# Kernel tuning notes

Measured on AMD Instinct MI355X. Metric: run time of the kernel, lower is better.

The kernel has to match this reference:

```python
import jax, jax.numpy as jnp
import numpy as np

N, B = 128, 8                                # seq_len, batch
V, E, H, S, T = 32000, 256, 256, 256, 32     # vocab, embed, hidden, segment_dim, segment_threshold


def _gru_cell(x, h, Wi, Wh, bi, bh):
    # PyTorch GRU cell convention (gates ordered r,z,n)
    gi = x @ Wi.T + bi
    gh = h @ Wh.T + bh
    ir, iz, inn = jnp.split(gi, 3, axis=-1)
    hr, hz, hn = jnp.split(gh, 3, axis=-1)
    r = jax.nn.sigmoid(ir + hr)
    z = jax.nn.sigmoid(iz + hz)
    n = jnp.tanh(inn + r * hn)
    return (1.0 - z) * n + z * h


def _run_gru(xs, h0, Wi, Wh, bi, bh):
    def step(h, x):
        h = _gru_cell(x, h, Wi, Wh, bi, bh)
        return h, h
    hT, ys = jax.lax.scan(step, h0, xs)
    return ys, hT


def setup_inputs() -> dict:
    key = jax.random.key(0)
    ks = jax.random.split(key, 17)
    sc = 1.0 / np.sqrt(H).astype(np.float32)
    w = lambda k, shape: jax.random.normal(k, shape, jnp.float32) * sc
    return {
        "tokens": jax.random.randint(ks[0], (N, B), 0, V, dtype=jnp.int32),
        "emb": w(ks[1], (V, E)),
        "Wi_f": w(ks[2], (3 * H, E)), "Wh_f": w(ks[3], (3 * H, H)),
        "bi_f": w(ks[4], (3 * H,)),  "bh_f": w(ks[5], (3 * H,)),
        "Wi_r": w(ks[6], (3 * H, E)), "Wh_r": w(ks[7], (3 * H, H)),
        "bi_r": w(ks[8], (3 * H,)),  "bh_r": w(ks[9], (3 * H,)),
        "Wi_s": w(ks[10], (3 * S, 2 * H)), "Wh_s": w(ks[11], (3 * S, S)),
        "bi_s": w(ks[12], (3 * S,)), "bh_s": w(ks[13], (3 * S,)),
        # deterministic stand-ins for the per-start torch.randn initial hiddens
        "h0f": jax.random.normal(ks[14], (N, B, S), jnp.float32),
        "h0b": jax.random.normal(ks[15], (N, B, S), jnp.float32),
    }


def reference(tokens, emb, Wi_f, Wh_f, bi_f, bh_f, Wi_r, Wh_r, bi_r, bh_r,
              Wi_s, Wh_s, bi_s, bh_s, h0f, h0b):
    x = emb[tokens]                                   # (N,B,E); dropout p=0
    h0 = jnp.zeros((B, H), x.dtype)
    ys_f, _ = _run_gru(x, h0, Wi_f, Wh_f, bi_f, bh_f)
    ys_r, _ = _run_gru(x[::-1], h0, Wi_r, Wh_r, bi_r, bh_r)
    outputs = jnp.concatenate([ys_f, ys_r[::-1]], axis=-1)   # (N,B,2H)

    def seg(window, h0i):                             # window (T,B,2H)
        def step(h, xt):
            h = _gru_cell(xt, h, Wi_s, Wh_s, bi_s, bh_s)
            return h, h
        hT, ys = jax.lax.scan(step, h0i, window)
        return ys, hT

    ii = jnp.arange(N)[:, None]                       # (N,1) segment start i
    tt = jnp.arange(T)[None, :]                       # (1,T) step within window
    jf = ii + tt                                      # forward target column j
    jb = ii - tt                                      # backward target row j
    win_f = outputs[jnp.clip(jf, 0, N - 1)]           # (N,T,B,2H)
    win_b = outputs[jnp.clip(jb, 0, N - 1)]
    outs_f, _ = jax.vmap(seg)(win_f, h0f)             # (N,T,B,S)
    outs_b, hT_b = jax.vmap(seg)(win_b, h0b)

    jf_s = jnp.where(jf < N, jf, N)                   # OOB index -> dropped
    jb_s = jnp.where(jb >= 0, jb, N)
    dp_f = jnp.zeros((N, N, B, S), outputs.dtype).at[ii, jf_s].set(outs_f, mode="drop")
    dp_b = jnp.zeros((N, N, B, S), outputs.dtype).at[jb_s, ii].set(outs_b, mode="drop")
    dp = jnp.concatenate([dp_f, dp_b], axis=-1)       # (N,N,B,2S)
    rows, cols = jnp.triu_indices(N)
    dp_tri = dp[rows, cols]                           # (N*(N+1)/2, B, 2S)

    # final hiddens as the torch loops leave them: forward i=N-1 runs exactly
    # one step; backward i=N-1 runs T steps (N >= T so all in range).
    hid_f = _gru_cell(outputs[-1], h0f[-1], Wi_s, Wh_s, bi_s, bh_s)
    hidden = jnp.concatenate([hid_f, hT_b[-1]], axis=-1)[None]  # (1,B,2S)
    return dp_tri, hidden
```

## Files before the change

### kernel.cpp

```cpp
#include <hip/hip_runtime.h>
#include <cstdint>
#include <cstddef>

#define NN 128
#define BB 8
#define EE 256
#define HH 256
#define SS 256
#define TT 32
#define G3 768
#define HBSTR 264
#define HIDOFF 33816576ull
#define OUT_ELEMS 33820672ull

typedef __attribute__((ext_vector_type(8))) short bf16x8;
typedef __attribute__((ext_vector_type(4))) float f32x4;
typedef __attribute__((ext_vector_type(4))) unsigned u32x4;
typedef _Float16 f16;
typedef __attribute__((ext_vector_type(2))) _Float16 f16x2;

__device__ __forceinline__ float bf2f(unsigned short u) {
    union { unsigned u; float f; } v; v.u = ((unsigned)u) << 16; return v.f;
}
__device__ __forceinline__ unsigned short f2bf(float f) {
    union { float f; unsigned u; } v; v.f = f;
    unsigned r = v.u + 0x7fffu + ((v.u >> 16) & 1u);
    return (unsigned short)(r >> 16);
}
__device__ __forceinline__ unsigned short f2h(float f) {
    union { f16 h; unsigned short u; } v; v.h = (f16)f; return v.u;
}
__device__ __forceinline__ float dot2h(unsigned wu, unsigned hu, float acc) {
    union { unsigned u; f16x2 h; } a, b2;
    a.u = wu; b2.u = hu;
    return __builtin_amdgcn_fdot2(a.h, b2.h, acc, false);
}
__device__ __forceinline__ float rcpf(float x) { return __builtin_amdgcn_rcpf(x); }
__device__ __forceinline__ float sigm(float x) { return rcpf(1.f + __expf(-x)); }
__device__ __forceinline__ float tanh_fast(float x) {
    float xc = fminf(fmaxf(x, -10.f), 10.f);
    float e2 = __expf(2.f * xc);
    return (e2 - 1.f) * rcpf(e2 + 1.f);
}

__device__ __forceinline__ int detect_f32(const void* emb) {
    const unsigned* w = (const unsigned*)emb;
    int bad = 0;
    for (int i = 0; i < 128; ++i) {
        unsigned u = w[i];
        bad |= (((u >> 7)  & 0xFFu) >= 0xC8u);
        bad |= (((u >> 23) & 0xFFu) >= 0xC8u);
    }
    return bad;
}
__device__ __forceinline__ float lds1(const void* p, size_t i, int f32) {
    return f32 ? ((const float*)p)[i] : bf2f(((const unsigned short*)p)[i]);
}
__device__ __forceinline__ void outw(void* p, size_t i, float v, int f32) {
    if (f32) ((float*)p)[i] = v;
    else ((unsigned short*)p)[i] = f2bf(v);
}

__global__ __launch_bounds__(256) void conv_all(
    const void* __restrict__ Wi_f, const void* __restrict__ Wi_r,
    const void* __restrict__ Wh_f, const void* __restrict__ Wh_r,
    const void* __restrict__ Wh_s, const void* __restrict__ Wi_s,
    unsigned short* __restrict__ dst, const void* __restrict__ emb) {
    const int f32 = detect_f32(emb);
    size_t i = ((size_t)blockIdx.x * 256 + threadIdx.x) * 8;
    const void* src; size_t off; int h16 = 0;
    if      (i < 196608)  { src = Wi_f; off = i; }
    else if (i < 393216)  { src = Wi_r; off = i - 196608; }
    else if (i < 589824)  { src = Wh_f; off = i - 393216; h16 = 1; }
    else if (i < 786432)  { src = Wh_r; off = i - 589824; h16 = 1; }
    else if (i < 983040)  { src = Wh_s; off = i - 786432; }
    else                  { src = Wi_s; off = i - 983040; }
    bf16x8 v;
    if (f32) {
        const float* q = (const float*)src + off;
        float4 a = *(const float4*)q, b4 = *(const float4*)(q + 4);
        float f[8] = {a.x, a.y, a.z, a.w, b4.x, b4.y, b4.z, b4.w};
#pragma unroll
        for (int j = 0; j < 8; ++j)
            v[j] = (short)(h16 ? f2h(f[j]) : f2bf(f[j]));
    } else {
        v = *(const bf16x8*)((const unsigned short*)src + off);
        if (h16) {
#pragma unroll
            for (int j = 0; j < 8; ++j)
                v[j] = (short)f2h(bf2f((unsigned short)v[j]));
        }
    }
    *(bf16x8*)(dst + i) = v;
}

template <int KK>
__global__ __launch_bounds__(256) void gemm_mfma(
    const int* __restrict__ tok, const void* __restrict__ Asrc,
    const unsigned short* __restrict__ W,  const void* __restrict__ bias,
    unsigned short* __restrict__ C,
    const unsigned short* __restrict__ W2, const void* __restrict__ bias2,
    unsigned short* __restrict__ C2, const void* __restrict__ emb) {

    const int f32 = detect_f32(emb);
    __shared__ unsigned short As[64 * 260];

    int bid = blockIdx.x;
    const unsigned short* Wp = W; const void* bp = bias; unsigned short* Cp = C;
    if (C2 && bid >= 128) { bid -= 128; Wp = W2; bp = bias2; Cp = C2; }
    const int mb = bid >> 3, nb = bid & 7;

    const int tid = threadIdx.x, wave = tid >> 6, lane = tid & 63;
    const int l15 = lane & 15, quad = lane >> 4;

    f32x4 acc[6];
#pragma unroll
    for (int nt = 0; nt < 6; ++nt) acc[nt] = (f32x4){0.f, 0.f, 0.f, 0.f};

    for (int kh = 0; kh < KK; kh += 256) {
        __syncthreads();
        for (int e = tid * 4; e < 64 * 256; e += 1024) {
            int r = e >> 8, k = e & 255;
            int gr = mb * 64 + r;
            unsigned short h4[4];
            if (tok) {
                size_t arow = (size_t)tok[gr] * EE + kh + k;
                if (f32) {
                    float4 v = *(const float4*)((const float*)Asrc + arow);
                    h4[0] = f2bf(v.x); h4[1] = f2bf(v.y); h4[2] = f2bf(v.z); h4[3] = f2bf(v.w);
                } else {
                    *(uint2*)h4 = *(const uint2*)((const unsigned short*)Asrc + arow);
                }
            } else {
                *(uint2*)h4 = *(const uint2*)((const unsigned short*)Asrc + (size_t)gr * KK + kh + k);
            }
            *(uint2*)(As + r * 260 + k) = *(uint2*)h4;
        }
        __syncthreads();
#pragma unroll
        for (int kt = 0; kt < 8; ++kt) {
            bf16x8 Af = *(const bf16x8*)(As + (wave * 16 + l15) * 260 + kt * 32 + quad * 8);
#pragma unroll
            for (int nt = 0; nt < 6; ++nt) {
                int col = nb * 96 + nt * 16 + l15;
                bf16x8 Bfr = *(const bf16x8*)(Wp + (size_t)col * KK + kh + kt * 32 + quad * 8);
                acc[nt] = __builtin_amdgcn_mfma_f32_16x16x32_bf16(Af, Bfr, acc[nt], 0, 0, 0);
            }
        }
    }
#pragma unroll
    for (int nt = 0; nt < 6; ++nt) {
        int col = nb * 96 + nt * 16 + l15;
        float bv = lds1(bp, col, f32);
#pragma unroll
        for (int r4 = 0; r4 < 4; ++r4) {
            int row = mb * 64 + wave * 16 + quad * 4 + r4;
            Cp[(size_t)row * G3 + col] = f2bf(acc[nt][r4] + bv);
        }
    }
}

__global__ __attribute__((amdgpu_flat_work_group_size(512, 512), amdgpu_waves_per_eu(2, 2)))
void token_scan_zero(
    const unsigned short* __restrict__ gi_f, const unsigned short* __restrict__ gi_r,
    const unsigned short* __restrict__ Wh_fh, const unsigned short* __restrict__ Wh_rh,
    const void* __restrict__ bh_f, const void* __restrict__ bh_r,
    unsigned short* __restrict__ outp, void* __restrict__ dout,
    const void* __restrict__ emb) {

    const int f32 = detect_f32(emb);

    if (blockIdx.x >= 16) {
        u32x4 z = (u32x4){0u, 0u, 0u, 0u};
        u32x4* p = (u32x4*)dout;
        const size_t nvec = OUT_ELEMS * (f32 ? 4 : 2) / 16;
        size_t stride = (size_t)(gridDim.x - 16) * 512;
        for (size_t v = (size_t)(blockIdx.x - 16) * 512 + threadIdx.x; v < nvec; v += stride)
            __builtin_nontemporal_store(z, p + v);
        return;
    }

    const int dir = blockIdx.x & 1;
    const int b   = blockIdx.x >> 1;
    const int tid = threadIdx.x;
    const int c = tid & 255, kh = tid >> 8;

    __shared__ __align__(16) unsigned short hbs[256];
    __shared__ float pr[3][256];

    const unsigned short* Wh = dir ? Wh_rh : Wh_fh;
    const unsigned short* gi = dir ? gi_r : gi_f;
    const void* bh = dir ? bh_r : bh_f;

    unsigned w[192];
#pragma unroll
    for (int g = 0; g < 3; ++g) {
        const unsigned* wp = (const unsigned*)(Wh + (size_t)(g * 256 + c) * 256 + kh * 128);
#pragma unroll
        for (int q = 0; q < 16; ++q) {
            uint4 v = *(const uint4*)(wp + q * 4);
            w[g * 64 + q * 4 + 0] = v.x; w[g * 64 + q * 4 + 1] = v.y;
            w[g * 64 + q * 4 + 2] = v.z; w[g * 64 + q * 4 + 3] = v.w;
        }
    }
#pragma unroll
    for (int i = 0; i < 192; ++i) asm volatile("" : "+v"(w[i]));

    const float bh0 = lds1(bh, c, f32);
    const float bh1 = lds1(bh, c + 256, f32);
    const float bh2 = lds1(bh, c + 512, f32);

    if (tid < 256) hbs[tid] = 0;
    float hreg = 0.f;
    __syncthreads();

    const unsigned* hbw = (const unsigned*)hbs + kh * 64;
    for (int t = 0; t < NN; ++t) {
        const int row = dir ? (NN - 1 - t) : t;
        unsigned short g0 = 0, g1 = 0, g2 = 0;
        if (kh == 0) {
            const unsigned short* gp = gi + (size_t)row * BB * G3 + (size_t)b * G3;
            g0 = gp[c]; g1 = gp[c + 256]; g2 = gp[c + 512];
        }
        float a0 = 0.f, a1 = 0.f, a2 = 0.f;
#pragma unroll
        for (int q = 0; q < 16; ++q) {
            uint4 hv = *(const uint4*)(hbw + q * 4);
            a0 = dot2h(w[      q * 4 + 0], hv.x, a0);
            a0 = dot2h(w[      q * 4 + 1], hv.y, a0);
            a0 = dot2h(w[      q * 4 + 2], hv.z, a0);
            a0 = dot2h(w[      q * 4 + 3], hv.w, a0);
            a1 = dot2h(w[ 64 + q * 4 + 0], hv.x, a1);
            a1 = dot2h(w[ 64 + q * 4 + 1], hv.y, a1);
            a1 = dot2h(w[ 64 + q * 4 + 2], hv.z, a1);
            a1 = dot2h(w[ 64 + q * 4 + 3], hv.w, a1);
            a2 = dot2h(w[128 + q * 4 + 0], hv.x, a2);
            a2 = dot2h(w[128 + q * 4 + 1], hv.y, a2);
            a2 = dot2h(w[128 + q * 4 + 2], hv.z, a2);
            a2 = dot2h(w[128 + q * 4 + 3], hv.w, a2);
        }
        if (kh) { pr[0][c] = a0; pr[1][c] = a1; pr[2][c] = a2; }
        __syncthreads();
        if (kh == 0) {
            a0 += pr[0][c]; a1 += pr[1][c]; a2 += pr[2][c];
            float rr = sigm(bf2f(g0) + a0 + bh0);
            float zz = sigm(bf2f(g1) + a1 + bh1);
            float nn = tanh_fast(bf2f(g2) + rr * (a2 + bh2));
            float hn = (1.f - zz) * nn + zz * hreg;
            hreg = hn;
            hbs[c] = f2h(hn);
        }
        __syncthreads();
        if (kh == 0)
            outp[((size_t)(row * BB + b)) * 512 + dir * 256 + c] = f2bf(hreg);
    }
}

__global__ __attribute__((amdgpu_flat_work_group_size(256, 256), amdgpu_waves_per_eu(1, 1)))
void seg_scan(
    const unsigned short* __restrict__ gi,
    const unsigned short* __restrict__ Whc,
    const void* __restrict__ bh,
    const void* __restrict__ h0f, const void* __restrict__ h0b,
    void* __restrict__ dout, const void* __restrict__ emb) {

    const int f32 = detect_f32(emb);

    __shared__ float gh[BB][G3];
    __shared__ __align__(16) unsigned short hb[16 * HBSTR];

    const int tid = threadIdx.x;
    const int wave = tid >> 6, lane = tid & 63;
    const int l15 = lane & 15, quad = lane >> 4;
    const int dir = blockIdx.x & 1, i0 = blockIdx.x >> 1;

    bf16x8 Ba[8][8]; bf16x8 Bv[8][4];
#pragma unroll
    for (int nt = 0; nt < 12; ++nt) {
        int col = wave * 192 + nt * 16 + l15;
#pragma unroll
        for (int kt = 0; kt < 8; ++kt) {
            bf16x8 f = *(const bf16x8*)(Whc + (size_t)col * 256 + kt * 32 + quad * 8);
            if (nt < 8) Ba[kt][nt] = f; else Bv[kt][nt - 8] = f;
        }
    }
#pragma unroll
    for (int kt = 0; kt < 8; ++kt) {
#pragma unroll
        for (int nt = 0; nt < 8; ++nt) asm volatile("" : "+a"(Ba[kt][nt]));
#pragma unroll
        for (int nt = 0; nt < 4; ++nt) asm volatile("" : "+v"(Bv[kt][nt]));
    }

    const void* h0 = dir ? h0b : h0f;
    const size_t h0base = (size_t)i0 * (BB * SS);
    const int c = tid;
    const float bh0 = lds1(bh, c, f32);
    const float bh1 = lds1(bh, c + 256, f32);
    const float bh2 = lds1(bh, c + 512, f32);
    float hreg[BB];
#pragma unroll
    for (int b = 0; b < BB; ++b) {
        float v = lds1(h0, h0base + b * 256 + c, f32);
        hreg[b] = v;
        hb[b * HBSTR + c] = f2bf(v);
    }
    for (int e = 8 * HBSTR + tid; e < 16 * HBSTR; e += 256) hb[e] = 0;
    __syncthreads();

    const int nsteps = dir ? min(TT, i0 + 1) : min(TT, NN - i0);
    for (int t = 0; t < nsteps; ++t) {
        const int j = dir ? (i0 - t) : (i0 + t);
        unsigned short gpre[BB][3];
        const unsigned short* gp = gi + (size_t)j * BB * G3;
#pragma unroll
        for (int b = 0; b < BB; ++b) {
            gpre[b][0] = gp[b * G3 + c];
            gpre[b][1] = gp[b * G3 + c + 256];
            gpre[b][2] = gp[b * G3 + c + 512];
        }
        {
            f32x4 acc[12];
#pragma unroll
            for (int nt = 0; nt < 12; ++nt) acc[nt] = (f32x4){0.f, 0.f, 0.f, 0.f};
#pragma unroll
            for (int kt = 0; kt < 8; ++kt) {
                bf16x8 Af = *(const bf16x8*)(hb + l15 * HBSTR + kt * 32 + quad * 8);
#pragma unroll
                for (int nt = 0; nt < 8; ++nt)
                    acc[nt] = __builtin_amdgcn_mfma_f32_16x16x32_bf16(Af, Ba[kt][nt], acc[nt], 0, 0, 0);
#pragma unroll
                for (int nt = 0; nt < 4; ++nt)
                    acc[8 + nt] = __builtin_amdgcn_mfma_f32_16x16x32_bf16(Af, Bv[kt][nt], acc[8 + nt], 0, 0, 0);
            }
            if (quad < 2) {
#pragma unroll
                for (int nt = 0; nt < 12; ++nt) {
                    int col = wave * 192 + nt * 16 + l15;
#pragma unroll
                    for (int r4 = 0; r4 < 4; ++r4) gh[quad * 4 + r4][col] = acc[nt][r4];
                }
            }
        }
        __syncthreads();

#pragma unroll
        for (int b = 0; b < BB; ++b) {
            float rr = sigm(bf2f(gpre[b][0]) + gh[b][c] + bh0);
            float zz = sigm(bf2f(gpre[b][1]) + gh[b][c + 256] + bh1);
            float nn = tanh_fast(bf2f(gpre[b][2]) + rr * (gh[b][c + 512] + bh2));
            float hn = (1.f - zz) * nn + zz * hreg[b];
            hreg[b] = hn;
            hb[b * HBSTR + c] = f2bf(hn);
        }
        __syncthreads();

        const int r0 = dir ? j : i0;
        const size_t tri = (size_t)r0 * NN - (size_t)(r0 * (r0 - 1)) / 2 + t;
        const size_t obase = tri * (BB * 512) + (dir ? 256 : 0);
#pragma unroll
        for (int b = 0; b < BB; ++b) {
            outw(dout, obase + b * 512 + c, hreg[b], f32);
            if (i0 == NN - 1) {
                if (dir == 0 && t == 0)      outw(dout, HIDOFF + b * 512 + c, hreg[b], f32);
                if (dir == 1 && t == TT - 1) outw(dout, HIDOFF + 256 + b * 512 + c, hreg[b], f32);
            }
        }
    }
}

extern "C" void kernel_launch(void* const* d_in, const int* in_sizes, int n_in,
                              void* d_out, int out_size, void* d_ws, size_t ws_size,
                              hipStream_t stream) {
    const int* tokens = (const int*)d_in[0];
    const void* emb   = d_in[1];
    const void* Wi_f  = d_in[2];
    const void* Wh_f  = d_in[3];
    const void* bi_f  = d_in[4];
    const void* bh_f  = d_in[5];
    const void* Wi_r  = d_in[6];
    const void* Wh_r  = d_in[7];
    const void* bi_r  = d_in[8];
    const void* bh_r  = d_in[9];
    const void* Wi_s  = d_in[10];
    const void* Wh_s  = d_in[11];
    const void* bi_s  = d_in[12];
    const void* bh_s  = d_in[13];
    const void* h0f   = d_in[14];
    const void* h0b   = d_in[15];

    unsigned short* wsu = (unsigned short*)d_ws;
    unsigned short* gif  = wsu;
    unsigned short* gir  = wsu + 786432;
    unsigned short* outp = wsu + 1572864;
    unsigned short* wcv  = wsu + 2097152;
    unsigned short* gis  = gif;

    const unsigned short* Wi_fc = wcv;
    const unsigned short* Wi_rc = wcv + 196608;
    const unsigned short* Wh_fh = wcv + 393216;
    const unsigned short* Wh_rh = wcv + 589824;
    const unsigned short* Wh_sc = wcv + 786432;
    const unsigned short* Wi_sc = wcv + 983040;

    conv_all<<<dim3(672), dim3(256), 0, stream>>>(Wi_f, Wi_r, Wh_f, Wh_r, Wh_s, Wi_s,
                                                  wcv, emb);
    gemm_mfma<256><<<dim3(256), dim3(256), 0, stream>>>(
        tokens, emb, Wi_fc, bi_f, gif, Wi_rc, bi_r, gir, emb);
    token_scan_zero<<<dim3(256), dim3(512), 0, stream>>>(gif, gir, Wh_fh, Wh_rh,
                                                         bh_f, bh_r, outp, d_out, emb);
    gemm_mfma<512><<<dim3(128), dim3(256), 0, stream>>>(
        nullptr, outp, Wi_sc, bi_s, gis, nullptr, nullptr, nullptr, emb);
    seg_scan<<<dim3(256), dim3(256), 0, stream>>>(gis, Wh_sc, bh_s, h0f, h0b, d_out, emb);
}
```

Measured before the change: 505.9 us.

## Split token GRU scan over four K-quarters and stream weights from cache

Changes the bidirectional token scan from 512 threads holding 192 weight registers each to 1024 threads that each cover a quarter of the K dimension. Weights are no longer pinned in registers; they are reloaded from global memory (L1/L2) on every timestep. Partial sums from three of the four quarters go through a larger LDS buffer. This shortens the serial dot-product chain per step, at the cost of repeated weight loads on the latency-critical recurrence. The zero-fill blocks also use the wider 1024-thread stride.

```diff
diff --git a/kernel.cpp b/kernel.cpp
--- a/kernel.cpp
+++ b/kernel.cpp
@@ -160,7 +160,7 @@
     }
 }
 
-__global__ __attribute__((amdgpu_flat_work_group_size(512, 512), amdgpu_waves_per_eu(2, 2)))
+__global__ __attribute__((amdgpu_flat_work_group_size(1024, 1024)))
 void token_scan_zero(
     const unsigned short* __restrict__ gi_f, const unsigned short* __restrict__ gi_r,
     const unsigned short* __restrict__ Wh_fh, const unsigned short* __restrict__ Wh_rh,
@@ -174,8 +174,8 @@
         u32x4 z = (u32x4){0u, 0u, 0u, 0u};
         u32x4* p = (u32x4*)dout;
         const size_t nvec = OUT_ELEMS * (f32 ? 4 : 2) / 16;
-        size_t stride = (size_t)(gridDim.x - 16) * 512;
-        for (size_t v = (size_t)(blockIdx.x - 16) * 512 + threadIdx.x; v < nvec; v += stride)
+        size_t stride = (size_t)(gridDim.x - 16) * 1024;
+        for (size_t v = (size_t)(blockIdx.x - 16) * 1024 + threadIdx.x; v < nvec; v += stride)
             __builtin_nontemporal_store(z, p + v);
         return;
     }
@@ -183,66 +183,62 @@
     const int dir = blockIdx.x & 1;
     const int b   = blockIdx.x >> 1;
     const int tid = threadIdx.x;
-    const int c = tid & 255, kh = tid >> 8;
+    const int c = tid & 255, kq = tid >> 8;
 
     __shared__ __align__(16) unsigned short hbs[256];
-    __shared__ float pr[3][256];
+    __shared__ float pr[3][3][256];
 
     const unsigned short* Wh = dir ? Wh_rh : Wh_fh;
     const unsigned short* gi = dir ? gi_r : gi_f;
     const void* bh = dir ? bh_r : bh_f;
 
-    unsigned w[192];
-#pragma unroll
-    for (int g = 0; g < 3; ++g) {
-        const unsigned* wp = (const unsigned*)(Wh + (size_t)(g * 256 + c) * 256 + kh * 128);
-#pragma unroll
-        for (int q = 0; q < 16; ++q) {
-            uint4 v = *(const uint4*)(wp + q * 4);
-            w[g * 64 + q * 4 + 0] = v.x; w[g * 64 + q * 4 + 1] = v.y;
-            w[g * 64 + q * 4 + 2] = v.z; w[g * 64 + q * 4 + 3] = v.w;
-        }
-    }
-#pragma unroll
-    for (int i = 0; i < 192; ++i) asm volatile("" : "+v"(w[i]));
-
-    const float bh0 = lds1(bh, c, f32);
-    const float bh1 = lds1(bh, c + 256, f32);
-    const float bh2 = lds1(bh, c + 512, f32);
+    const u32x4* wp0 = (const u32x4*)(Wh + (size_t)(0 * 256 + c) * 256 + kq * 64);
+    const u32x4* wp1 = (const u32x4*)(Wh + (size_t)(1 * 256 + c) * 256 + kq * 64);
+    const u32x4* wp2 = (const u32x4*)(Wh + (size_t)(2 * 256 + c) * 256 + kq * 64);
+
+    float bh0 = 0.f, bh1 = 0.f, bh2 = 0.f;
+    if (kq == 0) {
+        bh0 = lds1(bh, c, f32);
+        bh1 = lds1(bh, c + 256, f32);
+        bh2 = lds1(bh, c + 512, f32);
+    }
 
     if (tid < 256) hbs[tid] = 0;
     float hreg = 0.f;
     __syncthreads();
 
-    const unsigned* hbw = (const unsigned*)hbs + kh * 64;
+    const u32x4* hb4 = (const u32x4*)hbs + kq * 8;
     for (int t = 0; t < NN; ++t) {
         const int row = dir ? (NN - 1 - t) : t;
         unsigned short g0 = 0, g1 = 0, g2 = 0;
-        if (kh == 0) {
+        if (kq == 0) {
             const unsigned short* gp = gi + (size_t)row * BB * G3 + (size_t)b * G3;
             g0 = gp[c]; g1 = gp[c + 256]; g2 = gp[c + 512];
         }
         float a0 = 0.f, a1 = 0.f, a2 = 0.f;
 #pragma unroll
-        for (int q = 0; q < 16; ++q) {
-            uint4 hv = *(const uint4*)(hbw + q * 4);
-            a0 = dot2h(w[      q * 4 + 0], hv.x, a0);
-            a0 = dot2h(w[      q * 4 + 1], hv.y, a0);
-            a0 = dot2h(w[      q * 4 + 2], hv.z, a0);
-            a0 = dot2h(w[      q * 4 + 3], hv.w, a0);
-            a1 = dot2h(w[ 64 + q * 4 + 0], hv.x, a1);
-            a1 = dot2h(w[ 64 + q * 4 + 1], hv.y, a1);
-            a1 = dot2h(w[ 64 + q * 4 + 2], hv.z, a1);
-            a1 = dot2h(w[ 64 + q * 4 + 3], hv.w, a1);
-            a2 = dot2h(w[128 + q * 4 + 0], hv.x, a2);
-            a2 = dot2h(w[128 + q * 4 + 1], hv.y, a2);
-            a2 = dot2h(w[128 + q * 4 + 2], hv.z, a2);
-            a2 = dot2h(w[128 + q * 4 + 3], hv.w, a2);
-        }
-        if (kh) { pr[0][c] = a0; pr[1][c] = a1; pr[2][c] = a2; }
-        __syncthreads();
-        if (kh == 0) {
-            a0 += pr[0][c]; a1 += pr[1][c]; a2 += pr[2][c];
+        for (int q = 0; q < 8; ++q) {
+            u32x4 hv = hb4[q];
+            u32x4 w0 = wp0[q], w1 = wp1[q], w2 = wp2[q];
+            a0 = dot2h(w0[0], hv[0], a0);
+            a0 = dot2h(w0[1], hv[1], a0);
+            a0 = dot2h(w0[2], hv[2], a0);
+            a0 = dot2h(w0[3], hv[3], a0);
+            a1 = dot2h(w1[0], hv[0], a1);
+            a1 = dot2h(w1[1], hv[1], a1);
+            a1 = dot2h(w1[2], hv[2], a1);
+            a1 = dot2h(w1[3], hv[3], a1);
+            a2 = dot2h(w2[0], hv[0], a2);
+            a2 = dot2h(w2[1], hv[1], a2);
+            a2 = dot2h(w2[2], hv[2], a2);
+            a2 = dot2h(w2[3], hv[3], a2);
+        }
+        if (kq) { pr[kq - 1][0][c] = a0; pr[kq - 1][1][c] = a1; pr[kq - 1][2][c] = a2; }
+        __syncthreads();
+        if (kq == 0) {
+            a0 += pr[0][0][c] + pr[1][0][c] + pr[2][0][c];
+            a1 += pr[0][1][c] + pr[1][1][c] + pr[2][1][c];
+            a2 += pr[0][2][c] + pr[1][2][c] + pr[2][2][c];
             float rr = sigm(bf2f(g0) + a0 + bh0);
             float zz = sigm(bf2f(g1) + a1 + bh1);
             float nn = tanh_fast(bf2f(g2) + rr * (a2 + bh2));
@@ -251,7 +247,7 @@
             hbs[c] = f2h(hn);
         }
         __syncthreads();
-        if (kh == 0)
+        if (kq == 0)
             outp[((size_t)(row * BB + b)) * 512 + dir * 256 + c] = f2bf(hreg);
     }
 }
@@ -407,8 +403,8 @@
                                                   wcv, emb);
     gemm_mfma<256><<<dim3(256), dim3(256), 0, stream>>>(
         tokens, emb, Wi_fc, bi_f, gif, Wi_rc, bi_r, gir, emb);
-    token_scan_zero<<<dim3(256), dim3(512), 0, stream>>>(gif, gir, Wh_fh, Wh_rh,
-                                                         bh_f, bh_r, outp, d_out, emb);
+    token_scan_zero<<<dim3(256), dim3(1024), 0, stream>>>(gif, gir, Wh_fh, Wh_rh,
+                                                          bh_f, bh_r, outp, d_out, emb);
     gemm_mfma<512><<<dim3(128), dim3(256), 0, stream>>>(
         nullptr, outp, Wi_sc, bi_s, gis, nullptr, nullptr, nullptr, emb);
     seg_scan<<<dim3(256), dim3(256), 0, stream>>>(gis, Wh_sc, bh_s, h0f, h0b, d_out, emb);
```

Result: slower. 533.4 us (+5.4%).

## Merge forward and backward segment scans into one block filling all MFMA rows

Applied to the files above, without the earlier changes.

seg_scan now handles both directions for a start index in a single block, packing 8 forward and 8 backward batch rows into the 16-row MFMA tile that was previously half zero padding. This halves the grid to 128 blocks and removes the wasted MFMA rows. Each block pays for more gate math, and the steps run to the longer of the two directions with clamped indices. Separately, the token scan stops caching Wh in 192 registers and reloads the weights from global/cache every step, trading register pressure for repeated memory traffic.

```diff
diff --git a/kernel.cpp b/kernel.cpp
--- a/kernel.cpp
+++ b/kernel.cpp
@@ -192,19 +192,9 @@
     const unsigned short* gi = dir ? gi_r : gi_f;
     const void* bh = dir ? bh_r : bh_f;
 
-    unsigned w[192];
-#pragma unroll
-    for (int g = 0; g < 3; ++g) {
-        const unsigned* wp = (const unsigned*)(Wh + (size_t)(g * 256 + c) * 256 + kh * 128);
-#pragma unroll
-        for (int q = 0; q < 16; ++q) {
-            uint4 v = *(const uint4*)(wp + q * 4);
-            w[g * 64 + q * 4 + 0] = v.x; w[g * 64 + q * 4 + 1] = v.y;
-            w[g * 64 + q * 4 + 2] = v.z; w[g * 64 + q * 4 + 3] = v.w;
-        }
-    }
-#pragma unroll
-    for (int i = 0; i < 192; ++i) asm volatile("" : "+v"(w[i]));
+    const unsigned* wp0 = (const unsigned*)(Wh + (size_t)(0 * 256 + c) * 256 + kh * 128);
+    const unsigned* wp1 = (const unsigned*)(Wh + (size_t)(1 * 256 + c) * 256 + kh * 128);
+    const unsigned* wp2 = (const unsigned*)(Wh + (size_t)(2 * 256 + c) * 256 + kh * 128);
 
     const float bh0 = lds1(bh, c, f32);
     const float bh1 = lds1(bh, c + 256, f32);
@@ -214,7 +204,7 @@
     float hreg = 0.f;
     __syncthreads();
 
-    const unsigned* hbw = (const unsigned*)hbs + kh * 64;
+    const u32x4* hb4 = (const u32x4*)hbs + kh * 16;
     for (int t = 0; t < NN; ++t) {
         const int row = dir ? (NN - 1 - t) : t;
         unsigned short g0 = 0, g1 = 0, g2 = 0;
@@ -225,19 +215,22 @@
         float a0 = 0.f, a1 = 0.f, a2 = 0.f;
 #pragma unroll
         for (int q = 0; q < 16; ++q) {
-            uint4 hv = *(const uint4*)(hbw + q * 4);
-            a0 = dot2h(w[      q * 4 + 0], hv.x, a0);
-            a0 = dot2h(w[      q * 4 + 1], hv.y, a0);
-            a0 = dot2h(w[      q * 4 + 2], hv.z, a0);
-            a0 = dot2h(w[      q * 4 + 3], hv.w, a0);
-            a1 = dot2h(w[ 64 + q * 4 + 0], hv.x, a1);
-            a1 = dot2h(w[ 64 + q * 4 + 1], hv.y, a1);
-            a1 = dot2h(w[ 64 + q * 4 + 2], hv.z, a1);
-            a1 = dot2h(w[ 64 + q * 4 + 3], hv.w, a1);
-            a2 = dot2h(w[128 + q * 4 + 0], hv.x, a2);
-            a2 = dot2h(w[128 + q * 4 + 1], hv.y, a2);
-            a2 = dot2h(w[128 + q * 4 + 2], hv.z, a2);
-            a2 = dot2h(w[128 + q * 4 + 3], hv.w, a2);
+            u32x4 hv = hb4[q];
+            u32x4 w0 = *(const u32x4*)(wp0 + q * 4);
+            u32x4 w1 = *(const u32x4*)(wp1 + q * 4);
+            u32x4 w2 = *(const u32x4*)(wp2 + q * 4);
+            a0 = dot2h(w0[0], hv[0], a0);
+            a0 = dot2h(w0[1], hv[1], a0);
+            a0 = dot2h(w0[2], hv[2], a0);
+            a0 = dot2h(w0[3], hv[3], a0);
+            a1 = dot2h(w1[0], hv[0], a1);
+            a1 = dot2h(w1[1], hv[1], a1);
+            a1 = dot2h(w1[2], hv[2], a1);
+            a1 = dot2h(w1[3], hv[3], a1);
+            a2 = dot2h(w2[0], hv[0], a2);
+            a2 = dot2h(w2[1], hv[1], a2);
+            a2 = dot2h(w2[2], hv[2], a2);
+            a2 = dot2h(w2[3], hv[3], a2);
         }
         if (kh) { pr[0][c] = a0; pr[1][c] = a1; pr[2][c] = a2; }
         __syncthreads();
@@ -266,13 +259,13 @@
 
     const int f32 = detect_f32(emb);
 
-    __shared__ float gh[BB][G3];
+    __shared__ float gh[16][G3];
     __shared__ __align__(16) unsigned short hb[16 * HBSTR];
 
     const int tid = threadIdx.x;
     const int wave = tid >> 6, lane = tid & 63;
     const int l15 = lane & 15, quad = lane >> 4;
-    const int dir = blockIdx.x & 1, i0 = blockIdx.x >> 1;
+    const int i0 = blockIdx.x;
 
     bf16x8 Ba[8][8]; bf16x8 Bv[8][4];
 #pragma unroll
@@ -292,78 +285,108 @@
         for (int nt = 0; nt < 4; ++nt) asm volatile("" : "+v"(Bv[kt][nt]));
     }
 
-    const void* h0 = dir ? h0b : h0f;
-    const size_t h0base = (size_t)i0 * (BB * SS);
     const int c = tid;
     const float bh0 = lds1(bh, c, f32);
     const float bh1 = lds1(bh, c + 256, f32);
     const float bh2 = lds1(bh, c + 512, f32);
-    float hreg[BB];
-#pragma unroll
-    for (int b = 0; b < BB; ++b) {
-        float v = lds1(h0, h0base + b * 256 + c, f32);
-        hreg[b] = v;
-        hb[b * HBSTR + c] = f2bf(v);
-    }
-    for (int e = 8 * HBSTR + tid; e < 16 * HBSTR; e += 256) hb[e] = 0;
+
+    const size_t h0base = (size_t)i0 * (BB * SS);
+    float hreg[16];
+#pragma unroll
+    for (int q = 0; q < 8; ++q) {
+        float v = lds1(h0f, h0base + q * 256 + c, f32);
+        hreg[q] = v;
+        hb[q * HBSTR + c] = f2bf(v);
+    }
+#pragma unroll
+    for (int q = 8; q < 16; ++q) {
+        float v = lds1(h0b, h0base + (q - 8) * 256 + c, f32);
+        hreg[q] = v;
+        hb[q * HBSTR + c] = f2bf(v);
+    }
     __syncthreads();
 
-    const int nsteps = dir ? min(TT, i0 + 1) : min(TT, NN - i0);
-    for (int t = 0; t < nsteps; ++t) {
-        const int j = dir ? (i0 - t) : (i0 + t);
-        unsigned short gpre[BB][3];
-        const unsigned short* gp = gi + (size_t)j * BB * G3;
-#pragma unroll
-        for (int b = 0; b < BB; ++b) {
-            gpre[b][0] = gp[b * G3 + c];
-            gpre[b][1] = gp[b * G3 + c + 256];
-            gpre[b][2] = gp[b * G3 + c + 512];
-        }
-        {
-            f32x4 acc[12];
-#pragma unroll
-            for (int nt = 0; nt < 12; ++nt) acc[nt] = (f32x4){0.f, 0.f, 0.f, 0.f};
+    const int nf = min(TT, NN - i0);
+    const int nb = min(TT, i0 + 1);
+    const int nT = nf > nb ? nf : nb;
+
+    for (int t = 0; t < nT; ++t) {
+        const int jf = min(i0 + t, NN - 1);
+        const int jb = max(i0 - t, 0);
+        unsigned short gpre[16][3];
+        const unsigned short* gpf = gi + (size_t)jf * BB * G3;
+        const unsigned short* gpb = gi + (size_t)jb * BB * G3;
+#pragma unroll
+        for (int q = 0; q < 8; ++q) {
+            gpre[q][0] = gpf[q * G3 + c];
+            gpre[q][1] = gpf[q * G3 + c + 256];
+            gpre[q][2] = gpf[q * G3 + c + 512];
+        }
+#pragma unroll
+        for (int q = 8; q < 16; ++q) {
+            gpre[q][0] = gpb[(q - 8) * G3 + c];
+            gpre[q][1] = gpb[(q - 8) * G3 + c + 256];
+            gpre[q][2] = gpb[(q - 8) * G3 + c + 512];
+        }
+#pragma unroll
+        for (int half = 0; half < 2; ++half) {
+            f32x4 acc[6];
+#pragma unroll
+            for (int n = 0; n < 6; ++n) acc[n] = (f32x4){0.f, 0.f, 0.f, 0.f};
 #pragma unroll
             for (int kt = 0; kt < 8; ++kt) {
                 bf16x8 Af = *(const bf16x8*)(hb + l15 * HBSTR + kt * 32 + quad * 8);
-#pragma unroll
-                for (int nt = 0; nt < 8; ++nt)
-                    acc[nt] = __builtin_amdgcn_mfma_f32_16x16x32_bf16(Af, Ba[kt][nt], acc[nt], 0, 0, 0);
-#pragma unroll
-                for (int nt = 0; nt < 4; ++nt)
-                    acc[8 + nt] = __builtin_amdgcn_mfma_f32_16x16x32_bf16(Af, Bv[kt][nt], acc[8 + nt], 0, 0, 0);
-            }
-            if (quad < 2) {
-#pragma unroll
-                for (int nt = 0; nt < 12; ++nt) {
-                    int col = wave * 192 + nt * 16 + l15;
-#pragma unroll
-                    for (int r4 = 0; r4 < 4; ++r4) gh[quad * 4 + r4][col] = acc[nt][r4];
+                if (half == 0) {
+#pragma unroll
+                    for (int n = 0; n < 6; ++n)
+                        acc[n] = __builtin_amdgcn_mfma_f32_16x16x32_bf16(Af, Ba[kt][n], acc[n], 0, 0, 0);
+                } else {
+                    acc[0] = __builtin_amdgcn_mfma_f32_16x16x32_bf16(Af, Ba[kt][6], acc[0], 0, 0, 0);
+                    acc[1] = __builtin_amdgcn_mfma_f32_16x16x32_bf16(Af, Ba[kt][7], acc[1], 0, 0, 0);
+#pragma unroll
+                    for (int n = 0; n < 4; ++n)
+                        acc[2 + n] = __builtin_amdgcn_mfma_f32_16x16x32_bf16(Af, Bv[kt][n], acc[2 + n], 0, 0, 0);
                 }
             }
-        }
-        __syncthreads();
-
-#pragma unroll
-        for (int b = 0; b < BB; ++b) {
-            float rr = sigm(bf2f(gpre[b][0]) + gh[b][c] + bh0);
-            float zz = sigm(bf2f(gpre[b][1]) + gh[b][c + 256] + bh1);
-            float nn = tanh_fast(bf2f(gpre[b][2]) + rr * (gh[b][c + 512] + bh2));
-            float hn = (1.f - zz) * nn + zz * hreg[b];
-            hreg[b] = hn;
-            hb[b * HBSTR + c] = f2bf(hn);
-        }
-        __syncthreads();
-
-        const int r0 = dir ? j : i0;
-        const size_t tri = (size_t)r0 * NN - (size_t)(r0 * (r0 - 1)) / 2 + t;
-        const size_t obase = tri * (BB * 512) + (dir ? 256 : 0);
-#pragma unroll
-        for (int b = 0; b < BB; ++b) {
-            outw(dout, obase + b * 512 + c, hreg[b], f32);
-            if (i0 == NN - 1) {
-                if (dir == 0 && t == 0)      outw(dout, HIDOFF + b * 512 + c, hreg[b], f32);
-                if (dir == 1 && t == TT - 1) outw(dout, HIDOFF + 256 + b * 512 + c, hreg[b], f32);
+#pragma unroll
+            for (int n = 0; n < 6; ++n) {
+                int col = wave * 192 + (half * 6 + n) * 16 + l15;
+#pragma unroll
+                for (int r4 = 0; r4 < 4; ++r4) gh[quad * 4 + r4][col] = acc[n][r4];
+            }
+        }
+        __syncthreads();
+
+#pragma unroll
+        for (int q = 0; q < 16; ++q) {
+            float rr = sigm(bf2f(gpre[q][0]) + gh[q][c] + bh0);
+            float zz = sigm(bf2f(gpre[q][1]) + gh[q][c + 256] + bh1);
+            float nn = tanh_fast(bf2f(gpre[q][2]) + rr * (gh[q][c + 512] + bh2));
+            float hn = (1.f - zz) * nn + zz * hreg[q];
+            hreg[q] = hn;
+            hb[q * HBSTR + c] = f2bf(hn);
+        }
+        __syncthreads();
+
+        if (t < nf) {
+            const size_t tri = (size_t)i0 * NN - (size_t)(i0 * (i0 - 1)) / 2 + t;
+            const size_t ob = tri * (BB * 512);
+#pragma unroll
+            for (int q = 0; q < 8; ++q) {
+                outw(dout, ob + q * 512 + c, hreg[q], f32);
+                if (i0 == NN - 1)
+                    outw(dout, HIDOFF + q * 512 + c, hreg[q], f32);
+            }
+        }
+        if (t < nb) {
+            const int r0 = i0 - t;
+            const size_t tri = (size_t)r0 * NN - (size_t)(r0 * (r0 - 1)) / 2 + t;
+            const size_t ob = tri * (BB * 512) + 256;
+#pragma unroll
+            for (int q = 8; q < 16; ++q) {
+                outw(dout, ob + (q - 8) * 512 + c, hreg[q], f32);
+                if (i0 == NN - 1 && t == TT - 1)
+                    outw(dout, HIDOFF + 256 + (q - 8) * 512 + c, hreg[q], f32);
             }
         }
     }
@@ -411,5 +434,5 @@
                                                          bh_f, bh_r, outp, d_out, emb);
     gemm_mfma<512><<<dim3(128), dim3(256), 0, stream>>>(
         nullptr, outp, Wi_sc, bi_s, gis, nullptr, nullptr, nullptr, emb);
-    seg_scan<<<dim3(256), dim3(256), 0, stream>>>(gis, Wh_sc, bh_s, h0f, h0b, d_out, emb);
-}
+    seg_scan<<<dim3(128), dim3(256), 0, stream>>>(gis, Wh_sc, bh_s, h0f, h0b, d_out, emb);
+}
```

After: 545.4 us. 1.08x slower.
